# Performance work log

Measured on AMD Instinct MI355X. Metric: run time of the kernel, lower is better.

## Reference

```python
import jax, jax.numpy as jnp
import numpy as np

N, E, D_IN, D_E, D, L, D_OUT = 20000, 320000, 64, 16, 256, 4, 10


def _gine(x, e, src, dst, eps, W1, b1, W2, b2):
    """GINE conv: MLP((1+eps)*x + sum_{j->i} relu(x_j + e_ji))."""
    msg = jax.nn.relu(x[src] + e)                                   # [E, D]
    agg = jax.ops.segment_sum(msg, dst, num_segments=x.shape[0])    # [N, D]
    h = (1.0 + eps) * x + agg
    return jax.nn.relu(h @ W1 + b1) @ W2 + b2


def setup_inputs() -> dict:
    key = jax.random.key(0)
    ks = jax.random.split(key, 24)
    p = lambda k, sh: jax.random.normal(k, sh, jnp.float32) * 0.05
    return {
        "x": jax.random.normal(ks[0], (N, D_IN), jnp.float32),
        "edge_attr": jax.random.normal(ks[1], (E, D_E), jnp.float32),
        "edge_index": jax.random.randint(ks[2], (2, E), 0, N, jnp.int32),
        # FeatureEncoder: node and edge linear encoders to dim_inner
        "W_ne": p(ks[3], (D_IN, D)), "b_ne": jnp.zeros((D,), jnp.float32),
        "W_ee": p(ks[4], (D_E, D)), "b_ee": jnp.zeros((D,), jnp.float32),
        # pre-MP: one Linear+ReLU layer
        "W_pre": p(ks[5], (D, D)), "b_pre": jnp.zeros((D,), jnp.float32),
        # GINEAggregation (k-hop agg module)
        "eps_a": jnp.zeros((), jnp.float32),
        "W1_a": p(ks[6], (D, D)), "b1_a": jnp.zeros((D,), jnp.float32),
        "W2_a": p(ks[7], (D, D)), "b2_a": jnp.zeros((D,), jnp.float32),
        # L stacked DelayGINEConvLayer params
        "eps_l": jnp.zeros((L,), jnp.float32),
        "W1_l": p(ks[8], (L, D, D)), "b1_l": jnp.zeros((L, D), jnp.float32),
        "W2_l": p(ks[9], (L, D, D)), "b2_l": jnp.zeros((L, D), jnp.float32),
        # head
        "W_h": p(ks[10], (D, D_OUT)), "b_h": jnp.zeros((D_OUT,), jnp.float32),
    }


def reference(x, edge_attr, edge_index, W_ne, b_ne, W_ee, b_ee, W_pre, b_pre,
              eps_a, W1_a, b1_a, W2_a, b2_a, eps_l, W1_l, b1_l, W2_l, b2_l,
              W_h, b_h):
    src, dst = edge_index[0], edge_index[1]
    # FeatureEncoder
    h = x @ W_ne + b_ne                                  # [N, D]
    e = edge_attr @ W_ee + b_ee                          # [E, D]
    # pre-MP
    h = jax.nn.relu(h @ W_pre + b_pre)
    # k-hop GINE aggregation module
    h = _gine(h, e, src, dst, eps_a, W1_a, b1_a, W2_a, b2_a)
    # stacked DelayGINE conv layers with residual connections
    for i in range(L):
        h = h + _gine(h, e, src, dst, eps_l[i], W1_l[i], b1_l[i], W2_l[i], b2_l[i])
    # node-level head
    return h @ W_h + b_h                                 # [N, D_OUT]
```

## Files before the change

### kernel.cpp

```cpp
#include <hip/hip_runtime.h>
#include <hip/hip_bf16.h>

namespace {

constexpr int NN = 20000;
constexpr int NE = 320000;
constexpr int DI = 64;
constexpr int DE = 16;
constexpr int DM = 256;
constexpr int DO = 10;

__host__ __device__ constexpr size_t woff(int m) {
  return m == 0 ? 0 : (size_t)16384 + (size_t)(m - 1) * 65536;
}
constexpr size_t WTOTAL = 16384 + 11 * 65536;

typedef __attribute__((ext_vector_type(8))) short s16x8;
typedef __attribute__((ext_vector_type(4))) float f32x4;
typedef __attribute__((ext_vector_type(2))) float f32x2;

#if __has_builtin(__builtin_amdgcn_cvt_pk_f32_fp8)
#define HWFP8 1
#else
#define HWFP8 0
#endif

__device__ inline unsigned short f2bf(float x) {
  union { float f; unsigned u; } c; c.f = x;
  unsigned r = (c.u + 0x7FFFu + ((c.u >> 16) & 1u)) >> 16;
  return (unsigned short)r;
}
__device__ inline float bf2f(unsigned short h) {
  union { unsigned u; float f; } c; c.u = ((unsigned)h) << 16;
  return c.f;
}

#if HWFP8
__device__ inline unsigned char f2e4m3(float x) {
  union { float f; unsigned u; } c; c.f = x;
  const unsigned s = (c.u >> 24) & 0x80u;
  c.u &= 0x7FFFFFFFu;
  c.f = fminf(c.f, 448.f);
  unsigned rn;
  if (c.f < 0.015625f) {
    rn = (unsigned)rintf(c.f * 512.0f);
  } else {
    const unsigned b = c.u + 0x7FFFFu + ((c.u >> 20) & 1u);
    rn = (b >> 20) - 960u;
  }
  return (unsigned char)(s | rn);
}
__device__ inline void dec8(uint2 ev, float* e) {
  const f32x2 d0 = __builtin_amdgcn_cvt_pk_f32_fp8((int)ev.x, false);
  const f32x2 d1 = __builtin_amdgcn_cvt_pk_f32_fp8((int)ev.x, true);
  const f32x2 d2 = __builtin_amdgcn_cvt_pk_f32_fp8((int)ev.y, false);
  const f32x2 d3 = __builtin_amdgcn_cvt_pk_f32_fp8((int)ev.y, true);
  e[0] = d0.x; e[1] = d0.y; e[2] = d1.x; e[3] = d1.y;
  e[4] = d2.x; e[5] = d2.y; e[6] = d3.x; e[7] = d3.y;
}
#else
__device__ inline unsigned char f2e4m3(float x) {
  union { float f; unsigned u; } c; c.f = x;
  const unsigned s = (c.u >> 24) & 0x80u;
  c.u &= 0x7FFFFFFFu;
  c.f = fminf(c.f, 448.f);
  const unsigned b = c.u + 0x7FFFFu + ((c.u >> 20) & 1u);
  unsigned r = (b >> 20) - 960u;
  r = (c.f >= 0.0078125f) ? r : 0u;
  return (unsigned char)(s | r);
}
__device__ inline float e4m32f(unsigned u) {
  unsigned b = ((u & 0x80u) << 24) | (((u & 0x7Fu) << 20) + 0x3C000000u);
  if ((u & 0x7Fu) == 0) b &= 0x80000000u;
  union { unsigned u; float f; } c; c.u = b;
  return c.f;
}
__device__ inline void dec8(uint2 ev, float* e) {
  #pragma unroll
  for (int k = 0; k < 4; ++k) {
    e[k]     = e4m32f((ev.x >> (8 * k)) & 255u);
    e[4 + k] = e4m32f((ev.y >> (8 * k)) & 255u);
  }
}
#endif


__global__ __launch_bounds__(256) void zero_kernel(int* __restrict__ p, int n) {
  const int j = blockIdx.x * 256 + threadIdx.x;
  if (j < n) p[j] = 0;
}

__global__ __launch_bounds__(256) void hist_kernel(
    const int* __restrict__ dst, int* __restrict__ counts, int E)
{
  const int j = blockIdx.x * 256 + threadIdx.x;
  if (j < E) atomicAdd(&counts[dst[j]], 1);
}

__global__ __launch_bounds__(1024) void scan_kernel(
    const int* __restrict__ counts, int* __restrict__ row_ptr,
    int* __restrict__ cursor, int n)
{
  __shared__ int partial[1024];
  const int t = threadIdx.x;
  const int chunk = (n + 1023) / 1024;
  const int beg = t * chunk;
  const int end = min(beg + chunk, n);
  int s = 0;
  for (int i = beg; i < end; ++i) s += counts[i];
  partial[t] = s;
  __syncthreads();
  for (int off = 1; off < 1024; off <<= 1) {
    const int v = (t >= off) ? partial[t - off] : 0;
    __syncthreads();
    partial[t] += v;
    __syncthreads();
  }
  int base = (t == 0) ? 0 : partial[t - 1];
  for (int i = beg; i < end; ++i) {
    const int c = counts[i];
    row_ptr[i] = base;
    cursor[i] = base;
    base += c;
  }
  if (t == 1023) row_ptr[n] = partial[1023];
}

__global__ __launch_bounds__(256) void scatter_kernel(
    const int* __restrict__ src, const int* __restrict__ dst,
    const float* __restrict__ eattr, int* __restrict__ cursor,
    int* __restrict__ esrc, unsigned short* __restrict__ ea16, int E)
{
  const int j = blockIdx.x * 256 + threadIdx.x;
  if (j < E) {
    const int p = atomicAdd(&cursor[dst[j]], 1);
    esrc[p] = src[j];
    const float4* ep = reinterpret_cast<const float4*>(&eattr[(size_t)j * DE]);
    const float4 e0 = ep[0], e1 = ep[1], e2 = ep[2], e3 = ep[3];
    const float ea[16] = {e0.x, e0.y, e0.z, e0.w, e1.x, e1.y, e1.z, e1.w,
                          e2.x, e2.y, e2.z, e2.w, e3.x, e3.y, e3.z, e3.w};
    s16x8 v0, v1;
    #pragma unroll
    for (int k = 0; k < 8; ++k) {
      v0[k] = (short)f2bf(ea[k]);
      v1[k] = (short)f2bf(ea[8 + k]);
    }
    s16x8* op = reinterpret_cast<s16x8*>(&ea16[(size_t)p * DE]);
    op[0] = v0; op[1] = v1;
  }
}

__global__ __launch_bounds__(256) void convertW_kernel(
    const float* __restrict__ W_ne, const float* __restrict__ W_pre,
    const float* __restrict__ W1_a, const float* __restrict__ W2_a,
    const float* __restrict__ W1_l, const float* __restrict__ W2_l,
    unsigned short* __restrict__ hi)
{
  const int mat = blockIdx.y;
  const float* src;
  int K = 256;
  if (mat == 0)      { src = W_ne;  K = 64; }
  else if (mat == 1) { src = W_pre; }
  else if (mat == 2) { src = W1_a; }
  else if (mat == 3) { src = W2_a; }
  else if (mat < 8)  { src = W1_l + (size_t)(mat - 4) * 65536; }
  else               { src = W2_l + (size_t)(mat - 8) * 65536; }
  const size_t off = woff(mat);

  const int ntiles = (K >> 6) * 4;
  const int t = blockIdx.x;
  if (t >= ntiles) return;
  const int tk = t % (K >> 6);
  const int tn = t / (K >> 6);

  __shared__ float tile[64][65];
  const int tid = threadIdx.x;
  const int c = tid & 63;
  const int rg = tid >> 6;
  for (int i = 0; i < 16; ++i) {
    const int r = rg + i * 4;
    tile[r][c] = src[(size_t)(tk * 64 + r) * 256 + tn * 64 + c];
  }
  __syncthreads();
  const int k = tk * 64 + c;
  for (int i = 0; i < 16; ++i) {
    const int nn = rg + i * 4;
    const int n = tn * 64 + nn;
    hi[off + (size_t)n * K + k] = f2bf(tile[c][nn]);
  }
}

__global__ __launch_bounds__(256) void convertWee_kernel(
    const float* __restrict__ Wee, unsigned short* __restrict__ Wt16)
{
  const int n = threadIdx.x;
  #pragma unroll
  for (int k = 0; k < DE; ++k)
    Wt16[n * DE + k] = f2bf(Wee[k * DM + n]);
}

__global__ __launch_bounds__(256) void eenc_kernel(
    const unsigned short* __restrict__ ea16, const unsigned short* __restrict__ Wt16,
    const float* __restrict__ bee, unsigned char* __restrict__ e8)
{
  __shared__ unsigned char stage[128][144];
  const int tid = threadIdx.x;
  const int lane = tid & 63, wid = tid >> 6;
  const int l15 = lane & 15, l4 = lane >> 4;
  const int eBase0 = blockIdx.x * 128;
  const int eBase = eBase0 + wid * 32;
  const int colBase = blockIdx.y * 128;
  const s16x8 zz = {0, 0, 0, 0, 0, 0, 0, 0};

  s16x8 ah[2];
  #pragma unroll
  for (int mi = 0; mi < 2; ++mi) {
    const int edge = eBase + mi * 16 + l15;
    ah[mi] = (l4 < 2)
        ? *reinterpret_cast<const s16x8*>(&ea16[(size_t)edge * DE + l4 * 8]) : zz;
  }
  s16x8 bh[8];
  #pragma unroll
  for (int ni = 0; ni < 8; ++ni) {
    const int col = colBase + ni * 16 + l15;
    bh[ni] = (l4 < 2)
        ? *reinterpret_cast<const s16x8*>(&Wt16[col * DE + l4 * 8]) : zz;
  }
  f32x4 acc[2][8];
  #pragma unroll
  for (int mi = 0; mi < 2; ++mi)
    #pragma unroll
    for (int ni = 0; ni < 8; ++ni)
      acc[mi][ni] = (f32x4){0.f, 0.f, 0.f, 0.f};
  #pragma unroll
  for (int mi = 0; mi < 2; ++mi)
    #pragma unroll
    for (int ni = 0; ni < 8; ++ni)
      acc[mi][ni] = __builtin_amdgcn_mfma_f32_16x16x32_bf16(ah[mi], bh[ni], acc[mi][ni], 0, 0, 0);

  #pragma unroll
  for (int ni = 0; ni < 8; ++ni) {
    const int col = ni * 16 + l15;
    const float bv = bee[colBase + col];
    #pragma unroll
    for (int mi = 0; mi < 2; ++mi) {
      #pragma unroll
      for (int r = 0; r < 4; ++r) {
        const int erow = wid * 32 + mi * 16 + l4 * 4 + r;
        stage[erow][col] = f2e4m3(acc[mi][ni][r] + bv);
      }
    }
  }
  __syncthreads();
  #pragma unroll
  for (int it = 0; it < 4; ++it) {
    const int idx = tid + it * 256;
    const int e = idx >> 3, cc = idx & 7;
    const s16x8 v = *reinterpret_cast<const s16x8*>(&stage[e][cc * 16]);
    *reinterpret_cast<s16x8*>(&e8[(size_t)(eBase0 + e) * DM + colBase + cc * 16]) = v;
  }
}

template<bool RELU1, bool RELU2, bool RESID, bool ABF16>
__global__ __launch_bounds__(512) void mlp_kernel(
    const float* __restrict__ Af, const unsigned short* __restrict__ Ab,
    const unsigned short* __restrict__ B1, const float* __restrict__ b1,
    const unsigned short* __restrict__ B2, const float* __restrict__ b2,
    unsigned short* __restrict__ O16, int M, int K1)
{
  __shared__ unsigned short Tst[64 * 256];
  __shared__ unsigned short Ws[256 * 32];
  unsigned short* Ast = Tst;

  const int tid = threadIdx.x;
  const int lane = tid & 63, wid = tid >> 6;
  const int wr = wid >> 2, wc = wid & 3;
  const int l15 = lane & 15, l4 = lane >> 4;
  const int rowBase = blockIdx.x * 64;
  const int colW = wc * 64;

  f32x4 acc[2][4];
  #pragma unroll
  for (int i = 0; i < 2; ++i)
    #pragma unroll
    for (int j = 0; j < 4; ++j) acc[i][j] = (f32x4){0.f, 0.f, 0.f, 0.f};

  const int nk1 = K1 >> 5;
  for (int ks = 0; ks < nk1; ++ks) {
    if (tid < 256) {
      const int row = tid >> 2, kc = tid & 3;
      const int grow = rowBase + row;
      const int chunk = row * 4 + (kc ^ (row & 3));
      s16x8 v = {0, 0, 0, 0, 0, 0, 0, 0};
      if (grow < M) {
        if (ABF16) {
          v = *reinterpret_cast<const s16x8*>(&Ab[(size_t)grow * K1 + ks * 32 + kc * 8]);
        } else {
          const float* p = Af + (size_t)grow * K1 + ks * 32 + kc * 8;
          const float4 v0 = *reinterpret_cast<const float4*>(p);
          const float4 v1 = *reinterpret_cast<const float4*>(p + 4);
          const float xs[8] = {v0.x, v0.y, v0.z, v0.w, v1.x, v1.y, v1.z, v1.w};
          #pragma unroll
          for (int j = 0; j < 8; ++j) v[j] = (short)f2bf(xs[j]);
        }
      }
      ((s16x8*)Ast)[chunk] = v;
    }
    #pragma unroll
    for (int i = 0; i < 2; ++i) {
      const int u = tid + i * 512;
      const int c = u >> 2, kc = u & 3;
      const int chunk = c * 4 + (kc ^ (c & 3));
      ((s16x8*)Ws)[chunk] = *reinterpret_cast<const s16x8*>(B1 + (size_t)c * K1 + ks * 32 + kc * 8);
    }
    __syncthreads();
    s16x8 a[2], bw[4];
    #pragma unroll
    for (int mi = 0; mi < 2; ++mi) {
      const int r = wr * 32 + mi * 16 + l15;
      a[mi] = ((const s16x8*)Ast)[r * 4 + (l4 ^ (r & 3))];
    }
    #pragma unroll
    for (int ni = 0; ni < 4; ++ni) {
      const int c = colW + ni * 16 + l15;
      bw[ni] = ((const s16x8*)Ws)[c * 4 + (l4 ^ (c & 3))];
    }
    #pragma unroll
    for (int mi = 0; mi < 2; ++mi)
      #pragma unroll
      for (int ni = 0; ni < 4; ++ni)
        acc[mi][ni] = __builtin_amdgcn_mfma_f32_16x16x32_bf16(a[mi], bw[ni], acc[mi][ni], 0, 0, 0);
    __syncthreads();
  }
  #pragma unroll
  for (int ni = 0; ni < 4; ++ni) {
    const int col = colW + ni * 16 + l15;
    const float bv = b1[col];
    #pragma unroll
    for (int mi = 0; mi < 2; ++mi) {
      #pragma unroll
      for (int r = 0; r < 4; ++r) {
        const int row = wr * 32 + mi * 16 + l4 * 4 + r;
        float v = acc[mi][ni][r] + bv;
        if (RELU1) v = fmaxf(v, 0.f);
        const int c32 = col >> 3;
        const int chunk = row * 32 + (c32 ^ (row & 31));
        Tst[chunk * 8 + (col & 7)] = f2bf(v);
        acc[mi][ni][r] = 0.f;
      }
    }
  }
  __syncthreads();

  for (int ks = 0; ks < 8; ++ks) {
    #pragma unroll
    for (int i = 0; i < 2; ++i) {
      const int u = tid + i * 512;
      const int c = u >> 2, kc = u & 3;
      const int chunk = c * 4 + (kc ^ (c & 3));
      ((s16x8*)Ws)[chunk] = *reinterpret_cast<const s16x8*>(B2 + (size_t)c * 256 + ks * 32 + kc * 8);
    }
    __syncthreads();
    s16x8 a[2], bw[4];
    #pragma unroll
    for (int mi = 0; mi < 2; ++mi) {
      const int row = wr * 32 + mi * 16 + l15;
      const int c32 = ks * 4 + l4;
      a[mi] = ((const s16x8*)Tst)[row * 32 + (c32 ^ (row & 31))];
    }
    #pragma unroll
    for (int ni = 0; ni < 4; ++ni) {
      const int c = colW + ni * 16 + l15;
      bw[ni] = ((const s16x8*)Ws)[c * 4 + (l4 ^ (c & 3))];
    }
    #pragma unroll
    for (int mi = 0; mi < 2; ++mi)
      #pragma unroll
      for (int ni = 0; ni < 4; ++ni)
        acc[mi][ni] = __builtin_amdgcn_mfma_f32_16x16x32_bf16(a[mi], bw[ni], acc[mi][ni], 0, 0, 0);
    __syncthreads();
  }
  #pragma unroll
  for (int ni = 0; ni < 4; ++ni) {
    const int gcol = colW + ni * 16 + l15;
    const float bv = b2[gcol];
    #pragma unroll
    for (int mi = 0; mi < 2; ++mi) {
      #pragma unroll
      for (int r = 0; r < 4; ++r) {
        const int grow = rowBase + wr * 32 + mi * 16 + l4 * 4 + r;
        if (grow < M) {
          float v = acc[mi][ni][r] + bv;
          if (RESID) v += bf2f(O16[(size_t)grow * DM + gcol]);
          if (RELU2) v = fmaxf(v, 0.f);
          O16[(size_t)grow * DM + gcol] = f2bf(v);
        }
      }
    }
  }
}

__global__ __launch_bounds__(256) void gather_e8_kernel(
    const unsigned short* __restrict__ h16,
    const int* __restrict__ row_ptr, const int* __restrict__ esrc,
    const unsigned char* __restrict__ e8,
    const float* __restrict__ eps_ptr, int eps_idx,
    unsigned short* __restrict__ out16, int n)
{
  const int tid = threadIdx.x;
  const int lane = tid & 63, wave = tid >> 6;
  const int half = lane >> 5;
  const int c8 = (lane & 31) * 8;
  const float ep1 = 1.0f + eps_ptr[eps_idx];
  const int stride = gridDim.x * 4;

  for (int i = blockIdx.x * 4 + wave; i < n; i += stride) {
    const int beg = row_ptr[i], end = row_ptr[i + 1];
    const int cnt = end - beg;
    float a[8];
    #pragma unroll
    for (int k = 0; k < 8; ++k) a[k] = 0.f;

    const int npair = cnt >> 1;
    int it = 0;
    for (; it + 4 <= npair; it += 4) {
      int pp[4], ss[4];
      #pragma unroll
      for (int j = 0; j < 4; ++j) {
        pp[j] = beg + 2 * (it + j) + half;
        ss[j] = esrc[pp[j]];
      }
      s16x8 hv[4]; uint2 ev[4];
      #pragma unroll
      for (int j = 0; j < 4; ++j) {
        hv[j] = *reinterpret_cast<const s16x8*>(&h16[(size_t)ss[j] * DM + c8]);
        ev[j] = *reinterpret_cast<const uint2*>(&e8[(size_t)pp[j] * DM + c8]);
      }
      #pragma unroll
      for (int j = 0; j < 4; ++j) {
        float ee[8];
        dec8(ev[j], ee);
        #pragma unroll
        for (int k = 0; k < 8; ++k)
          a[k] += fmaxf(bf2f((unsigned short)hv[j][k]) + ee[k], 0.f);
      }
    }
    for (; it < npair; ++it) {
      const int p0 = beg + 2 * it + half;
      const int s0 = esrc[p0];
      const s16x8 h0 = *reinterpret_cast<const s16x8*>(&h16[(size_t)s0 * DM + c8]);
      const uint2 e0 = *reinterpret_cast<const uint2*>(&e8[(size_t)p0 * DM + c8]);
      float ee[8];
      dec8(e0, ee);
      #pragma unroll
      for (int k = 0; k < 8; ++k)
        a[k] += fmaxf(bf2f((unsigned short)h0[k]) + ee[k], 0.f);
    }
    if ((cnt & 1) && half == 0) {
      const int p0 = end - 1;
      const int s0 = esrc[p0];
      const s16x8 h0 = *reinterpret_cast<const s16x8*>(&h16[(size_t)s0 * DM + c8]);
      const uint2 e0 = *reinterpret_cast<const uint2*>(&e8[(size_t)p0 * DM + c8]);
      float ee[8];
      dec8(e0, ee);
      #pragma unroll
      for (int k = 0; k < 8; ++k)
        a[k] += fmaxf(bf2f((unsigned short)h0[k]) + ee[k], 0.f);
    }
    #pragma unroll
    for (int k = 0; k < 8; ++k) a[k] += __shfl_xor(a[k], 32, 64);
    if (half == 0) {
      const s16x8 hs = *reinterpret_cast<const s16x8*>(&h16[(size_t)i * DM + c8]);
      s16x8 o;
      #pragma unroll
      for (int k = 0; k < 8; ++k)
        o[k] = (short)f2bf(ep1 * bf2f((unsigned short)hs[k]) + a[k]);
      *reinterpret_cast<s16x8*>(&out16[(size_t)i * DM + c8]) = o;
    }
  }
}

__global__ __launch_bounds__(256) void gather_rc_kernel(
    const unsigned short* __restrict__ h16,
    const int* __restrict__ row_ptr, const int* __restrict__ esrc,
    const unsigned short* __restrict__ ea16,
    const float* __restrict__ Wee, const float* __restrict__ bee,
    const float* __restrict__ eps_ptr, int eps_idx,
    unsigned short* __restrict__ out16, int n)
{
  const int tid = threadIdx.x;
  const int lane = tid & 63, wave = tid >> 6;
  const int c4 = lane * 4;
  float4 w[16];
  #pragma unroll
  for (int k = 0; k < 16; ++k)
    w[k] = *reinterpret_cast<const float4*>(&Wee[k * DM + c4]);
  const float4 bv = *reinterpret_cast<const float4*>(&bee[c4]);
  const float ep1 = 1.0f + eps_ptr[eps_idx];
  const int stride = gridDim.x * 4;

  for (int i = blockIdx.x * 4 + wave; i < n; i += stride) {
    const int beg = row_ptr[i], end = row_ptr[i + 1];
    float a0 = 0.f, a1 = 0.f, a2 = 0.f, a3 = 0.f;
    for (int p = beg; p < end; ++p) {
      const int s = esrc[p];
      const ushort4 hv = *reinterpret_cast<const ushort4*>(&h16[(size_t)s * DM + c4]);
      const s16x8* eap = reinterpret_cast<const s16x8*>(&ea16[(size_t)p * DE]);
      const s16x8 ew0 = eap[0], ew1 = eap[1];
      float m0 = bf2f(hv.x) + bv.x, m1 = bf2f(hv.y) + bv.y;
      float m2 = bf2f(hv.z) + bv.z, m3 = bf2f(hv.w) + bv.w;
      float ea[16];
      #pragma unroll
      for (int k = 0; k < 8; ++k) {
        ea[k] = bf2f((unsigned short)ew0[k]);
        ea[8 + k] = bf2f((unsigned short)ew1[k]);
      }
      #pragma unroll
      for (int k = 0; k < 16; ++k) {
        m0 += ea[k] * w[k].x; m1 += ea[k] * w[k].y;
        m2 += ea[k] * w[k].z; m3 += ea[k] * w[k].w;
      }
      a0 += fmaxf(m0, 0.f); a1 += fmaxf(m1, 0.f);
      a2 += fmaxf(m2, 0.f); a3 += fmaxf(m3, 0.f);
    }
    const ushort4 hs = *reinterpret_cast<const ushort4*>(&h16[(size_t)i * DM + c4]);
    ushort4 o;
    o.x = f2bf(ep1 * bf2f(hs.x) + a0); o.y = f2bf(ep1 * bf2f(hs.y) + a1);
    o.z = f2bf(ep1 * bf2f(hs.z) + a2); o.w = f2bf(ep1 * bf2f(hs.w) + a3);
    *reinterpret_cast<ushort4*>(&out16[(size_t)i * DM + c4]) = o;
  }
}

__global__ __launch_bounds__(256) void head_kernel(
    const unsigned short* __restrict__ h16, const float* __restrict__ W,
    const float* __restrict__ b, float* __restrict__ out, int M)
{
  __shared__ float Ws[DM * DO];
  const int tid = threadIdx.x;
  for (int i = tid; i < DM * DO; i += 256) Ws[i] = W[i];
  __syncthreads();
  const int r = tid >> 4;
  const int c = tid & 15;
  const int row = blockIdx.x * 16 + r;
  if (row < M && c < DO) {
    const unsigned short* hp = &h16[(size_t)row * DM];
    float acc = 0.f;
    #pragma unroll 8
    for (int k = 0; k < DM; ++k) acc += bf2f(hp[k]) * Ws[k * DO + c];
    out[(size_t)row * DO + c] = acc + b[c];
  }
}

}

extern "C" void kernel_launch(void* const* d_in, const int* in_sizes, int n_in,
                              void* d_out, int out_size, void* d_ws, size_t ws_size,
                              hipStream_t stream) {
  const float* x     = (const float*)d_in[0];
  const float* eattr = (const float*)d_in[1];
  const int*   eidx  = (const int*)d_in[2];
  const float* W_ne  = (const float*)d_in[3];
  const float* b_ne  = (const float*)d_in[4];
  const float* W_ee  = (const float*)d_in[5];
  const float* b_ee  = (const float*)d_in[6];
  const float* W_pre = (const float*)d_in[7];
  const float* b_pre = (const float*)d_in[8];
  const float* eps_a = (const float*)d_in[9];
  const float* W1_a  = (const float*)d_in[10];
  const float* b1_a  = (const float*)d_in[11];
  const float* W2_a  = (const float*)d_in[12];
  const float* b2_a  = (const float*)d_in[13];
  const float* eps_l = (const float*)d_in[14];
  const float* W1_l  = (const float*)d_in[15];
  const float* b1_l  = (const float*)d_in[16];
  const float* W2_l  = (const float*)d_in[17];
  const float* b2_l  = (const float*)d_in[18];
  const float* W_h   = (const float*)d_in[19];
  const float* b_h   = (const float*)d_in[20];

  const int* src = eidx;
  const int* dst = eidx + NE;

  char* wp = (char*)d_ws;
  unsigned short* h16   = (unsigned short*)wp; wp += (size_t)NN * DM * 2;
  unsigned short* agg16 = (unsigned short*)wp; wp += (size_t)NN * DM * 2;
  unsigned short* ea16  = (unsigned short*)wp; wp += (size_t)NE * DE * 2;
  unsigned short* wt    = (unsigned short*)wp; wp += WTOTAL * 2;
  unsigned short* wtee  = (unsigned short*)wp; wp += (size_t)DM * DE * 2;
  int* esrc    = (int*)wp;                     wp += (size_t)NE * 4;
  int* counts  = (int*)wp;                     wp += (size_t)NN * 4;
  int* row_ptr = (int*)wp;                     wp += (size_t)(NN + 1) * 4;
  int* cursor  = (int*)wp;                     wp += (size_t)NN * 4;
  wp = (char*)(((uintptr_t)wp + 15) & ~(uintptr_t)15);
  unsigned char* e8 = (unsigned char*)wp;
  const size_t need_e8 = (size_t)(wp - (char*)d_ws) + (size_t)NE * DM;
  const bool use_e8 = ws_size >= need_e8;

  zero_kernel<<<(NN + 255) / 256, 256, 0, stream>>>(counts, NN);
  hist_kernel<<<(NE + 255) / 256, 256, 0, stream>>>(dst, counts, NE);
  scan_kernel<<<1, 1024, 0, stream>>>(counts, row_ptr, cursor, NN);
  scatter_kernel<<<(NE + 255) / 256, 256, 0, stream>>>(
      src, dst, eattr, cursor, esrc, ea16, NE);

  convertW_kernel<<<dim3(16, 12), 256, 0, stream>>>(
      W_ne, W_pre, W1_a, W2_a, W1_l, W2_l, wt);
  convertWee_kernel<<<1, 256, 0, stream>>>(W_ee, wtee);

  if (use_e8)
    eenc_kernel<<<dim3(NE / 128, 2), 256, 0, stream>>>(ea16, wtee, b_ee, e8);

  const int mlpgrid = (NN + 63) / 64;

  mlp_kernel<false, true, false, false><<<mlpgrid, 512, 0, stream>>>(
      x, nullptr, wt + woff(0), b_ne, wt + woff(1), b_pre, h16, NN, DI);

  for (int layer = 0; layer < 5; ++layer) {
    const float* eps; int ei; const float *b1, *b2; size_t o1, o2;
    if (layer == 0) {
      eps = eps_a; ei = 0; b1 = b1_a; b2 = b2_a;
      o1 = woff(2); o2 = woff(3);
    } else {
      const int i = layer - 1;
      eps = eps_l; ei = i;
      b1 = b1_l + (size_t)i * DM; b2 = b2_l + (size_t)i * DM;
      o1 = woff(4 + i); o2 = woff(8 + i);
    }
    if (use_e8)
      gather_e8_kernel<<<5000, 256, 0, stream>>>(
          h16, row_ptr, esrc, e8, eps, ei, agg16, NN);
    else
      gather_rc_kernel<<<1280, 256, 0, stream>>>(
          h16, row_ptr, esrc, ea16, W_ee, b_ee, eps, ei, agg16, NN);
    if (layer == 0)
      mlp_kernel<true, false, false, true><<<mlpgrid, 512, 0, stream>>>(
          nullptr, agg16, wt + o1, b1, wt + o2, b2, h16, NN, DM);
    else
      mlp_kernel<true, false, true, true><<<mlpgrid, 512, 0, stream>>>(
          nullptr, agg16, wt + o1, b1, wt + o2, b2, h16, NN, DM);
  }

  head_kernel<<<(NN + 15) / 16, 256, 0, stream>>>(h16, W_h, b_h, (float*)d_out, NN);
}
```

Baseline: 460.4 us.

## Fuse edge gather-aggregation with GINE MLP and use hardware fp8 packing

Merges the per-layer edge gather/segment-sum kernel with the two-layer MLP kernel. Each 64-row block first aggregates its nodes' neighbour messages into swizzled shared memory, then runs both GEMMs from there, with ping-pong h buffers so the residual reads the old h. This removes the agg16 round trip through global memory and one launch per layer. The cost is that the gather now runs at the MLP's grid and occupancy, where before it had its own 5000-block grid. Edge encoding also swaps to a transposed MFMA layout so it can write packed dwords using the hardware fp8 convert instruction.

Result: faster. 444.0 us (-3.6%).

```diff
diff --git a/kernel.cpp b/kernel.cpp
--- a/kernel.cpp
+++ b/kernel.cpp
@@ -19,7 +19,7 @@
 typedef __attribute__((ext_vector_type(4))) float f32x4;
 typedef __attribute__((ext_vector_type(2))) float f32x2;
 
-#if __has_builtin(__builtin_amdgcn_cvt_pk_f32_fp8)
+#if __has_builtin(__builtin_amdgcn_cvt_pk_f32_fp8) && __has_builtin(__builtin_amdgcn_cvt_pk_fp8_f32)
 #define HWFP8 1
 #else
 #define HWFP8 0
@@ -36,20 +36,6 @@
 }
 
 #if HWFP8
-__device__ inline unsigned char f2e4m3(float x) {
-  union { float f; unsigned u; } c; c.f = x;
-  const unsigned s = (c.u >> 24) & 0x80u;
-  c.u &= 0x7FFFFFFFu;
-  c.f = fminf(c.f, 448.f);
-  unsigned rn;
-  if (c.f < 0.015625f) {
-    rn = (unsigned)rintf(c.f * 512.0f);
-  } else {
-    const unsigned b = c.u + 0x7FFFFu + ((c.u >> 20) & 1u);
-    rn = (b >> 20) - 960u;
-  }
-  return (unsigned char)(s | rn);
-}
 __device__ inline void dec8(uint2 ev, float* e) {
   const f32x2 d0 = __builtin_amdgcn_cvt_pk_f32_fp8((int)ev.x, false);
   const f32x2 d1 = __builtin_amdgcn_cvt_pk_f32_fp8((int)ev.x, true);
@@ -203,7 +189,7 @@
     const unsigned short* __restrict__ ea16, const unsigned short* __restrict__ Wt16,
     const float* __restrict__ bee, unsigned char* __restrict__ e8)
 {
-  __shared__ unsigned char stage[128][144];
+  __shared__ unsigned stage_dw[128][36];
   const int tid = threadIdx.x;
   const int lane = tid & 63, wid = tid >> 6;
   const int l15 = lane & 15, l4 = lane >> 4;
@@ -226,37 +212,48 @@
     bh[ni] = (l4 < 2)
         ? *reinterpret_cast<const s16x8*>(&Wt16[col * DE + l4 * 8]) : zz;
   }
-  f32x4 acc[2][8];
-  #pragma unroll
-  for (int mi = 0; mi < 2; ++mi)
-    #pragma unroll
-    for (int ni = 0; ni < 8; ++ni)
-      acc[mi][ni] = (f32x4){0.f, 0.f, 0.f, 0.f};
-  #pragma unroll
-  for (int mi = 0; mi < 2; ++mi)
-    #pragma unroll
-    for (int ni = 0; ni < 8; ++ni)
-      acc[mi][ni] = __builtin_amdgcn_mfma_f32_16x16x32_bf16(ah[mi], bh[ni], acc[mi][ni], 0, 0, 0);
+  f32x4 acc2[8][2];
+  #pragma unroll
+  for (int ni = 0; ni < 8; ++ni)
+    #pragma unroll
+    for (int mi = 0; mi < 2; ++mi)
+      acc2[ni][mi] = (f32x4){0.f, 0.f, 0.f, 0.f};
+  #pragma unroll
+  for (int ni = 0; ni < 8; ++ni)
+    #pragma unroll
+    for (int mi = 0; mi < 2; ++mi)
+      acc2[ni][mi] = __builtin_amdgcn_mfma_f32_16x16x32_bf16(bh[ni], ah[mi], acc2[ni][mi], 0, 0, 0);
 
   #pragma unroll
   for (int ni = 0; ni < 8; ++ni) {
-    const int col = ni * 16 + l15;
-    const float bv = bee[colBase + col];
-    #pragma unroll
-    for (int mi = 0; mi < 2; ++mi) {
-      #pragma unroll
-      for (int r = 0; r < 4; ++r) {
-        const int erow = wid * 32 + mi * 16 + l4 * 4 + r;
-        stage[erow][col] = f2e4m3(acc[mi][ni][r] + bv);
-      }
+    const float4 bv = *reinterpret_cast<const float4*>(&bee[colBase + ni * 16 + l4 * 4]);
+    #pragma unroll
+    for (int mi = 0; mi < 2; ++mi) {
+      const int erow = wid * 32 + mi * 16 + l15;
+      const float v0 = acc2[ni][mi][0] + bv.x;
+      const float v1 = acc2[ni][mi][1] + bv.y;
+      const float v2 = acc2[ni][mi][2] + bv.z;
+      const float v3 = acc2[ni][mi][3] + bv.w;
+#if HWFP8
+      unsigned dw = 0;
+      dw = (unsigned)__builtin_amdgcn_cvt_pk_fp8_f32(v0, v1, (int)dw, false);
+      dw = (unsigned)__builtin_amdgcn_cvt_pk_fp8_f32(v2, v3, (int)dw, true);
+      stage_dw[erow][ni * 4 + l4] = dw;
+#else
+      unsigned char* bp = reinterpret_cast<unsigned char*>(&stage_dw[erow][0]);
+      const int col0 = ni * 16 + l4 * 4;
+      bp[col0 + 0] = f2e4m3(v0); bp[col0 + 1] = f2e4m3(v1);
+      bp[col0 + 2] = f2e4m3(v2); bp[col0 + 3] = f2e4m3(v3);
+#endif
     }
   }
   __syncthreads();
+  const unsigned char* sb = reinterpret_cast<const unsigned char*>(stage_dw);
   #pragma unroll
   for (int it = 0; it < 4; ++it) {
     const int idx = tid + it * 256;
     const int e = idx >> 3, cc = idx & 7;
-    const s16x8 v = *reinterpret_cast<const s16x8*>(&stage[e][cc * 16]);
+    const s16x8 v = *reinterpret_cast<const s16x8*>(sb + (size_t)e * 144 + cc * 16);
     *reinterpret_cast<s16x8*>(&e8[(size_t)(eBase0 + e) * DM + colBase + cc * 16]) = v;
   }
 }
@@ -400,82 +397,197 @@
   }
 }
 
-__global__ __launch_bounds__(256) void gather_e8_kernel(
-    const unsigned short* __restrict__ h16,
+template<bool RESID>
+__global__ __launch_bounds__(512) void gine_layer_kernel(
+    const unsigned short* __restrict__ h_in,
     const int* __restrict__ row_ptr, const int* __restrict__ esrc,
     const unsigned char* __restrict__ e8,
     const float* __restrict__ eps_ptr, int eps_idx,
-    unsigned short* __restrict__ out16, int n)
-{
+    const unsigned short* __restrict__ B1, const float* __restrict__ b1,
+    const unsigned short* __restrict__ B2, const float* __restrict__ b2,
+    unsigned short* __restrict__ h_out, int M)
+{
+  __shared__ unsigned short Tst[64 * 256];
+  __shared__ unsigned short Ws[256 * 32];
+
   const int tid = threadIdx.x;
-  const int lane = tid & 63, wave = tid >> 6;
-  const int half = lane >> 5;
-  const int c8 = (lane & 31) * 8;
+  const int lane = tid & 63, wid = tid >> 6;
+  const int wr = wid >> 2, wc = wid & 3;
+  const int l15 = lane & 15, l4 = lane >> 4;
+  const int rowBase = blockIdx.x * 64;
+  const int colW = wc * 64;
   const float ep1 = 1.0f + eps_ptr[eps_idx];
-  const int stride = gridDim.x * 4;
-
-  for (int i = blockIdx.x * 4 + wave; i < n; i += stride) {
-    const int beg = row_ptr[i], end = row_ptr[i + 1];
-    const int cnt = end - beg;
-    float a[8];
-    #pragma unroll
-    for (int k = 0; k < 8; ++k) a[k] = 0.f;
-
-    const int npair = cnt >> 1;
-    int it = 0;
-    for (; it + 4 <= npair; it += 4) {
-      int pp[4], ss[4];
-      #pragma unroll
-      for (int j = 0; j < 4; ++j) {
-        pp[j] = beg + 2 * (it + j) + half;
-        ss[j] = esrc[pp[j]];
-      }
-      s16x8 hv[4]; uint2 ev[4];
-      #pragma unroll
-      for (int j = 0; j < 4; ++j) {
-        hv[j] = *reinterpret_cast<const s16x8*>(&h16[(size_t)ss[j] * DM + c8]);
-        ev[j] = *reinterpret_cast<const uint2*>(&e8[(size_t)pp[j] * DM + c8]);
-      }
-      #pragma unroll
-      for (int j = 0; j < 4; ++j) {
+
+  {
+    const int half = lane >> 5;
+    const int c8 = (lane & 31) * 8;
+    for (int q = 0; q < 8; ++q) {
+      const int i = rowBase + wid * 8 + q;
+      if (i >= M) break;
+      const int beg = row_ptr[i], end = row_ptr[i + 1];
+      const int cnt = end - beg;
+      float a[8];
+      #pragma unroll
+      for (int k = 0; k < 8; ++k) a[k] = 0.f;
+
+      const int npair = cnt >> 1;
+      int it = 0;
+      for (; it + 4 <= npair; it += 4) {
+        int pp[4], ss[4];
+        #pragma unroll
+        for (int j = 0; j < 4; ++j) {
+          pp[j] = beg + 2 * (it + j) + half;
+          ss[j] = esrc[pp[j]];
+        }
+        s16x8 hv[4]; uint2 ev[4];
+        #pragma unroll
+        for (int j = 0; j < 4; ++j) {
+          hv[j] = *reinterpret_cast<const s16x8*>(&h_in[(size_t)ss[j] * DM + c8]);
+          ev[j] = *reinterpret_cast<const uint2*>(&e8[(size_t)pp[j] * DM + c8]);
+        }
+        #pragma unroll
+        for (int j = 0; j < 4; ++j) {
+          float ee[8];
+          dec8(ev[j], ee);
+          #pragma unroll
+          for (int k = 0; k < 8; ++k)
+            a[k] += fmaxf(bf2f((unsigned short)hv[j][k]) + ee[k], 0.f);
+        }
+      }
+      for (; it < npair; ++it) {
+        const int p0 = beg + 2 * it + half;
+        const int s0 = esrc[p0];
+        const s16x8 h0 = *reinterpret_cast<const s16x8*>(&h_in[(size_t)s0 * DM + c8]);
+        const uint2 e0 = *reinterpret_cast<const uint2*>(&e8[(size_t)p0 * DM + c8]);
         float ee[8];
-        dec8(ev[j], ee);
+        dec8(e0, ee);
         #pragma unroll
         for (int k = 0; k < 8; ++k)
-          a[k] += fmaxf(bf2f((unsigned short)hv[j][k]) + ee[k], 0.f);
-      }
-    }
-    for (; it < npair; ++it) {
-      const int p0 = beg + 2 * it + half;
-      const int s0 = esrc[p0];
-      const s16x8 h0 = *reinterpret_cast<const s16x8*>(&h16[(size_t)s0 * DM + c8]);
-      const uint2 e0 = *reinterpret_cast<const uint2*>(&e8[(size_t)p0 * DM + c8]);
-      float ee[8];
-      dec8(e0, ee);
-      #pragma unroll
-      for (int k = 0; k < 8; ++k)
-        a[k] += fmaxf(bf2f((unsigned short)h0[k]) + ee[k], 0.f);
-    }
-    if ((cnt & 1) && half == 0) {
-      const int p0 = end - 1;
-      const int s0 = esrc[p0];
-      const s16x8 h0 = *reinterpret_cast<const s16x8*>(&h16[(size_t)s0 * DM + c8]);
-      const uint2 e0 = *reinterpret_cast<const uint2*>(&e8[(size_t)p0 * DM + c8]);
-      float ee[8];
-      dec8(e0, ee);
-      #pragma unroll
-      for (int k = 0; k < 8; ++k)
-        a[k] += fmaxf(bf2f((unsigned short)h0[k]) + ee[k], 0.f);
-    }
-    #pragma unroll
-    for (int k = 0; k < 8; ++k) a[k] += __shfl_xor(a[k], 32, 64);
-    if (half == 0) {
-      const s16x8 hs = *reinterpret_cast<const s16x8*>(&h16[(size_t)i * DM + c8]);
-      s16x8 o;
-      #pragma unroll
-      for (int k = 0; k < 8; ++k)
-        o[k] = (short)f2bf(ep1 * bf2f((unsigned short)hs[k]) + a[k]);
-      *reinterpret_cast<s16x8*>(&out16[(size_t)i * DM + c8]) = o;
+          a[k] += fmaxf(bf2f((unsigned short)h0[k]) + ee[k], 0.f);
+      }
+      if ((cnt & 1) && half == 0) {
+        const int p0 = end - 1;
+        const int s0 = esrc[p0];
+        const s16x8 h0 = *reinterpret_cast<const s16x8*>(&h_in[(size_t)s0 * DM + c8]);
+        const uint2 e0 = *reinterpret_cast<const uint2*>(&e8[(size_t)p0 * DM + c8]);
+        float ee[8];
+        dec8(e0, ee);
+        #pragma unroll
+        for (int k = 0; k < 8; ++k)
+          a[k] += fmaxf(bf2f((unsigned short)h0[k]) + ee[k], 0.f);
+      }
+      #pragma unroll
+      for (int k = 0; k < 8; ++k) a[k] += __shfl_xor(a[k], 32, 64);
+      if (half == 0) {
+        const s16x8 hs = *reinterpret_cast<const s16x8*>(&h_in[(size_t)i * DM + c8]);
+        s16x8 o;
+        #pragma unroll
+        for (int k = 0; k < 8; ++k)
+          o[k] = (short)f2bf(ep1 * bf2f((unsigned short)hs[k]) + a[k]);
+        const int ln = wid * 8 + q;
+        const int c32 = lane & 31;
+        ((s16x8*)Tst)[ln * 32 + (c32 ^ (ln & 31))] = o;
+      }
+    }
+  }
+  __syncthreads();
+
+  f32x4 acc[2][4];
+  #pragma unroll
+  for (int i = 0; i < 2; ++i)
+    #pragma unroll
+    for (int j = 0; j < 4; ++j) acc[i][j] = (f32x4){0.f, 0.f, 0.f, 0.f};
+
+  for (int ks = 0; ks < 8; ++ks) {
+    #pragma unroll
+    for (int i = 0; i < 2; ++i) {
+      const int u = tid + i * 512;
+      const int c = u >> 2, kc = u & 3;
+      const int chunk = c * 4 + (kc ^ (c & 3));
+      ((s16x8*)Ws)[chunk] = *reinterpret_cast<const s16x8*>(B1 + (size_t)c * 256 + ks * 32 + kc * 8);
+    }
+    __syncthreads();
+    s16x8 a[2], bw[4];
+    #pragma unroll
+    for (int mi = 0; mi < 2; ++mi) {
+      const int r = wr * 32 + mi * 16 + l15;
+      const int c32 = ks * 4 + l4;
+      a[mi] = ((const s16x8*)Tst)[r * 32 + (c32 ^ (r & 31))];
+    }
+    #pragma unroll
+    for (int ni = 0; ni < 4; ++ni) {
+      const int c = colW + ni * 16 + l15;
+      bw[ni] = ((const s16x8*)Ws)[c * 4 + (l4 ^ (c & 3))];
+    }
+    #pragma unroll
+    for (int mi = 0; mi < 2; ++mi)
+      #pragma unroll
+      for (int ni = 0; ni < 4; ++ni)
+        acc[mi][ni] = __builtin_amdgcn_mfma_f32_16x16x32_bf16(a[mi], bw[ni], acc[mi][ni], 0, 0, 0);
+    __syncthreads();
+  }
+  #pragma unroll
+  for (int ni = 0; ni < 4; ++ni) {
+    const int col = colW + ni * 16 + l15;
+    const float bv = b1[col];
+    #pragma unroll
+    for (int mi = 0; mi < 2; ++mi) {
+      #pragma unroll
+      for (int r = 0; r < 4; ++r) {
+        const int row = wr * 32 + mi * 16 + l4 * 4 + r;
+        float v = fmaxf(acc[mi][ni][r] + bv, 0.f);
+        const int c32 = col >> 3;
+        const int chunk = row * 32 + (c32 ^ (row & 31));
+        Tst[chunk * 8 + (col & 7)] = f2bf(v);
+        acc[mi][ni][r] = 0.f;
+      }
+    }
+  }
+  __syncthreads();
+
+  for (int ks = 0; ks < 8; ++ks) {
+    #pragma unroll
+    for (int i = 0; i < 2; ++i) {
+      const int u = tid + i * 512;
+      const int c = u >> 2, kc = u & 3;
+      const int chunk = c * 4 + (kc ^ (c & 3));
+      ((s16x8*)Ws)[chunk] = *reinterpret_cast<const s16x8*>(B2 + (size_t)c * 256 + ks * 32 + kc * 8);
+    }
+    __syncthreads();
+    s16x8 a[2], bw[4];
+    #pragma unroll
+    for (int mi = 0; mi < 2; ++mi) {
+      const int row = wr * 32 + mi * 16 + l15;
+      const int c32 = ks * 4 + l4;
+      a[mi] = ((const s16x8*)Tst)[row * 32 + (c32 ^ (row & 31))];
+    }
+    #pragma unroll
+    for (int ni = 0; ni < 4; ++ni) {
+      const int c = colW + ni * 16 + l15;
+      bw[ni] = ((const s16x8*)Ws)[c * 4 + (l4 ^ (c & 3))];
+    }
+    #pragma unroll
+    for (int mi = 0; mi < 2; ++mi)
+      #pragma unroll
+      for (int ni = 0; ni < 4; ++ni)
+        acc[mi][ni] = __builtin_amdgcn_mfma_f32_16x16x32_bf16(a[mi], bw[ni], acc[mi][ni], 0, 0, 0);
+    __syncthreads();
+  }
+  #pragma unroll
+  for (int ni = 0; ni < 4; ++ni) {
+    const int gcol = colW + ni * 16 + l15;
+    const float bv = b2[gcol];
+    #pragma unroll
+    for (int mi = 0; mi < 2; ++mi) {
+      #pragma unroll
+      for (int r = 0; r < 4; ++r) {
+        const int grow = rowBase + wr * 32 + mi * 16 + l4 * 4 + r;
+        if (grow < M) {
+          float v = acc[mi][ni][r] + bv;
+          if (RESID) v += bf2f(h_in[(size_t)grow * DM + gcol]);
+          h_out[(size_t)grow * DM + gcol] = f2bf(v);
+        }
+      }
     }
   }
 }
@@ -582,7 +694,8 @@
   const int* dst = eidx + NE;
 
   char* wp = (char*)d_ws;
-  unsigned short* h16   = (unsigned short*)wp; wp += (size_t)NN * DM * 2;
+  unsigned short* hb0   = (unsigned short*)wp; wp += (size_t)NN * DM * 2;
+  unsigned short* hb1   = (unsigned short*)wp; wp += (size_t)NN * DM * 2;
   unsigned short* agg16 = (unsigned short*)wp; wp += (size_t)NN * DM * 2;
   unsigned short* ea16  = (unsigned short*)wp; wp += (size_t)NE * DE * 2;
   unsigned short* wt    = (unsigned short*)wp; wp += WTOTAL * 2;
@@ -612,7 +725,10 @@
   const int mlpgrid = (NN + 63) / 64;
 
   mlp_kernel<false, true, false, false><<<mlpgrid, 512, 0, stream>>>(
-      x, nullptr, wt + woff(0), b_ne, wt + woff(1), b_pre, h16, NN, DI);
+      x, nullptr, wt + woff(0), b_ne, wt + woff(1), b_pre, hb0, NN, DI);
+
+  unsigned short* hbuf[2] = {hb0, hb1};
+  int cur = 0;
 
   for (int layer = 0; layer < 5; ++layer) {
     const float* eps; int ei; const float *b1, *b2; size_t o1, o2;
@@ -625,19 +741,27 @@
       b1 = b1_l + (size_t)i * DM; b2 = b2_l + (size_t)i * DM;
       o1 = woff(4 + i); o2 = woff(8 + i);
     }
-    if (use_e8)
-      gather_e8_kernel<<<5000, 256, 0, stream>>>(
-          h16, row_ptr, esrc, e8, eps, ei, agg16, NN);
-    else
+    if (use_e8) {
+      if (layer == 0)
+        gine_layer_kernel<false><<<mlpgrid, 512, 0, stream>>>(
+            hbuf[cur], row_ptr, esrc, e8, eps, ei,
+            wt + o1, b1, wt + o2, b2, hbuf[cur ^ 1], NN);
+      else
+        gine_layer_kernel<true><<<mlpgrid, 512, 0, stream>>>(
+            hbuf[cur], row_ptr, esrc, e8, eps, ei,
+            wt + o1, b1, wt + o2, b2, hbuf[cur ^ 1], NN);
+      cur ^= 1;
+    } else {
       gather_rc_kernel<<<1280, 256, 0, stream>>>(
-          h16, row_ptr, esrc, ea16, W_ee, b_ee, eps, ei, agg16, NN);
-    if (layer == 0)
-      mlp_kernel<true, false, false, true><<<mlpgrid, 512, 0, stream>>>(
-          nullptr, agg16, wt + o1, b1, wt + o2, b2, h16, NN, DM);
-    else
-      mlp_kernel<true, false, true, true><<<mlpgrid, 512, 0, stream>>>(
-          nullptr, agg16, wt + o1, b1, wt + o2, b2, h16, NN, DM);
-  }
-
-  head_kernel<<<(NN + 15) / 16, 256, 0, stream>>>(h16, W_h, b_h, (float*)d_out, NN);
-}
+          hbuf[cur], row_ptr, esrc, ea16, W_ee, b_ee, eps, ei, agg16, NN);
+      if (layer == 0)
+        mlp_kernel<true, false, false, true><<<mlpgrid, 512, 0, stream>>>(
+            nullptr, agg16, wt + o1, b1, wt + o2, b2, hbuf[cur], NN, DM);
+      else
+        mlp_kernel<true, false, true, true><<<mlpgrid, 512, 0, stream>>>(
+            nullptr, agg16, wt + o1, b1, wt + o2, b2, hbuf[cur], NN, DM);
+    }
+  }
+
+  head_kernel<<<(NN + 15) / 16, 256, 0, stream>>>(hbuf[cur], W_h, b_h, (float*)d_out, NN);
+}
```
